# Optimization experiments

Hardware: AMD Instinct MI355X
Metric: run time of the kernel (lower is better)

Reference implementation:

```python
import jax, jax.numpy as jnp
import numpy as np

N = 200000          # graph_size (stalk rows)
H = 128             # hidden_channels
NNZ = 3200000       # Laplacian nnz (avg degree 16)
K = 15              # polynomial degree (poly_layers_K)
LAMBDA_MAX = 2.0    # normalised Laplacian -> analytic lambda_max


def setup_inputs() -> dict:
    key = jax.random.key(0)
    ks = jax.random.split(key, 6)
    x = jax.random.normal(ks[0], (N, H), dtype=jnp.float32)
    vals = jax.random.normal(ks[1], (NNZ,), dtype=jnp.float32)
    poly_logits = jax.random.normal(ks[2], (K + 1,), dtype=jnp.float32)
    hp_alpha = jax.random.normal(ks[3], (), dtype=jnp.float32)
    edge_row = jax.random.randint(ks[4], (NNZ,), 0, N, dtype=jnp.int64)
    edge_col = jax.random.randint(ks[5], (NNZ,), 0, N, dtype=jnp.int64)
    return {"x": x, "vals": vals, "poly_logits": poly_logits,
            "hp_alpha": hp_alpha, "edge_row": edge_row, "edge_col": edge_col}


def reference(x, vals, poly_logits, hp_alpha, edge_row, edge_col):
    n = x.shape[0]

    def spmm(v):  # (n,h) -> (n,h), sparse L @ v in COO form
        return jax.ops.segment_sum(vals[:, None] * v[edge_col], edge_row,
                                   num_segments=n)

    def Lhat(v):  # L_hat = (2/lambda_max) L - I
        return (2.0 / LAMBDA_MAX) * spmm(v) - v

    w = jax.nn.softmax(poly_logits)  # mixture over Chebyshev T_0..T_K

    # Chebyshev Type-1 recurrence: T_{k+1} = 2 L_hat T_k - T_{k-1}
    T0 = x
    T1 = Lhat(x)
    out = w[0] * T0 + w[1] * T1

    def step(carry, wk):
        T0, T1, out = carry
        Tk1 = 2.0 * Lhat(T1) - T0
        return (T1, Tk1, out + wk * Tk1), None

    (_, _, px), _ = jax.lax.scan(step, (T0, T1, out), w[2:])

    # high-pass term: x - (1/lambda_max) L x
    hp = x - spmm(x) / LAMBDA_MAX
    return -px + hp_alpha * hp
```

## Files before the change

kernel.cpp:

```cpp
#include <hip/hip_runtime.h>
#include <math.h>

#define N_NODES 200000
#define H_CH    128
#define GRP     64
#define NNZ_E   3200000
#define K_DEG   15

#define EPB     4096
#define BSHIFT  9
#define BROWS   512
#define NBUCK   391
#define BCAP    9216

__global__ void softmax_k(const float* __restrict__ logits, float* __restrict__ w) {
    if (threadIdx.x == 0) {
        float m = -1e30f;
        for (int i = 0; i <= K_DEG; ++i) m = fmaxf(m, logits[i]);
        float e[K_DEG + 1];
        float s = 0.f;
        for (int i = 0; i <= K_DEG; ++i) { e[i] = expf(logits[i] - m); s += e[i]; }
        float inv = 1.0f / s;
        for (int i = 0; i <= K_DEG; ++i) w[i] = e[i] * inv;
    }
}

__global__ __launch_bounds__(256) void bucketA_k(
    const int* __restrict__ row, const int* __restrict__ col,
    const float* __restrict__ vals,
    int* __restrict__ gfill, uint2* __restrict__ stag, int nnz) {
    __shared__ int cnt[NBUCK];
    __shared__ int excl[NBUCK];
    __shared__ int gbase[NBUCK];
    __shared__ int sm[256];
    __shared__ uint2 sstag[EPB];
    __shared__ unsigned short sb[EPB];

    int tid = threadIdx.x;
    int base = blockIdx.x * EPB;

    for (int t = tid; t < NBUCK; t += 256) cnt[t] = 0;
    __syncthreads();

    int r[16], c[16], b[16];
    float v[16];
#pragma unroll
    for (int j = 0; j < 16; ++j) {
        int i = base + j * 256 + tid;
        if (i < nnz) {
            r[j] = row[i]; c[j] = col[i]; v[j] = vals[i];
            b[j] = r[j] >> BSHIFT;
            atomicAdd(&cnt[b[j]], 1);
        } else {
            b[j] = -1;
        }
    }
    __syncthreads();

    {
        int b0 = 2 * tid, b1 = 2 * tid + 1;
        int c0 = (b0 < NBUCK) ? cnt[b0] : 0;
        int c1 = (b1 < NBUCK) ? cnt[b1] : 0;
        int pair = c0 + c1;
        sm[tid] = pair;
        __syncthreads();
        int incl = pair;
        for (int off = 1; off < 256; off <<= 1) {
            int tv = (tid >= off) ? sm[tid - off] : 0;
            __syncthreads();
            incl += tv;
            sm[tid] = incl;
            __syncthreads();
        }
        int pexcl = incl - pair;
        if (b0 < NBUCK) excl[b0] = pexcl;
        if (b1 < NBUCK) excl[b1] = pexcl + c0;
    }
    __syncthreads();

    for (int t = tid; t < NBUCK; t += 256) {
        int cb = cnt[t];
        gbase[t] = (cb > 0) ? atomicAdd(&gfill[t], cb) : 0;
    }
    __syncthreads();
    for (int t = tid; t < NBUCK; t += 256) cnt[t] = excl[t];
    __syncthreads();

#pragma unroll
    for (int j = 0; j < 16; ++j) {
        if (b[j] >= 0) {
            int p = atomicAdd(&cnt[b[j]], 1);
            sstag[p] = make_uint2(((unsigned)(r[j] & 511) << 18) | (unsigned)c[j],
                                  __float_as_uint(v[j]));
            sb[p] = (unsigned short)b[j];
        }
    }
    __syncthreads();

    int tot = nnz - base; if (tot > EPB) tot = EPB;
    for (int i = tid; i < tot; i += 256) {
        int bb = sb[i];
        size_t gp = (size_t)bb * BCAP + gbase[bb] + (i - excl[bb]);
        stag[gp] = sstag[i];
    }
}

__global__ void scanG_k(const int* __restrict__ gfill, int* __restrict__ bbase,
                        int* __restrict__ row_ptr) {
    __shared__ int sm[256];
    int tid = threadIdx.x;
    int j0 = 2 * tid, j1 = 2 * tid + 1;
    int c0 = (j0 < NBUCK) ? gfill[j0] : 0;
    int c1 = (j1 < NBUCK) ? gfill[j1] : 0;
    int pair = c0 + c1;
    sm[tid] = pair;
    __syncthreads();
    int incl = pair;
    for (int off = 1; off < 256; off <<= 1) {
        int t = (tid >= off) ? sm[tid - off] : 0;
        __syncthreads();
        incl += t;
        sm[tid] = incl;
        __syncthreads();
    }
    int pexcl = incl - pair;
    if (j0 < NBUCK) bbase[j0] = pexcl;
    if (j1 < NBUCK) bbase[j1] = pexcl + c0;
    if (tid == 0) row_ptr[N_NODES] = NNZ_E;
}

__global__ __launch_bounds__(256) void bucketB_k(
    const uint2* __restrict__ stag, const int* __restrict__ gfill,
    const int* __restrict__ bbase, int* __restrict__ row_ptr,
    int2* __restrict__ csr) {
    __shared__ int hist[BROWS];
    __shared__ int lexcl[BROWS];
    __shared__ int sm[256];
    int b = blockIdx.x;
    int n = gfill[b];
    int cs = bbase[b];
    const uint2* s = stag + (size_t)b * BCAP;
    int tid = threadIdx.x;

    hist[tid] = 0; hist[tid + 256] = 0;
    __syncthreads();
    for (int i = tid; i < n; i += 256)
        atomicAdd(&hist[s[i].x >> 18], 1);
    __syncthreads();

    int j0 = 2 * tid, j1 = 2 * tid + 1;
    int c0 = hist[j0], c1 = hist[j1];
    int pair = c0 + c1;
    sm[tid] = pair;
    __syncthreads();
    int incl = pair;
    for (int off = 1; off < 256; off <<= 1) {
        int t = (tid >= off) ? sm[tid - off] : 0;
        __syncthreads();
        incl += t;
        sm[tid] = incl;
        __syncthreads();
    }
    int pexcl = incl - pair;
    lexcl[j0] = pexcl;
    lexcl[j1] = pexcl + c0;

    int rbase = b << BSHIFT;
    if (rbase + j0 < N_NODES) row_ptr[rbase + j0] = cs + lexcl[j0];
    if (rbase + j1 < N_NODES) row_ptr[rbase + j1] = cs + lexcl[j1];
    hist[j0] = lexcl[j0];
    hist[j1] = lexcl[j1];
    __syncthreads();

    for (int i = tid; i < n; i += 256) {
        uint2 e = s[i];
        int rl = (int)(e.x >> 18);
        int p = cs + atomicAdd(&hist[rl], 1);
        int2 cv;
        cv.x = (int)(e.x & 0x3FFFF);
        cv.y = (int)e.y;
        csr[p] = cv;
    }
}

__global__ __launch_bounds__(256) void first_k(
    const int* __restrict__ rp, const int2* __restrict__ csr,
    const float* __restrict__ x, float* __restrict__ T1g, float* __restrict__ out,
    const float* __restrict__ w, const float* __restrict__ alpha_p, int goff) {
    int wid = blockIdx.x * 4 + (threadIdx.x >> 6);
    int r = __builtin_amdgcn_readfirstlane(wid);
    if (r >= N_NODES) return;
    int lane = threadIdx.x & 63;
    const float* base = x + goff + lane;
    int e0 = rp[r], e1 = rp[r + 1];
    float a0 = 0.f, a1 = 0.f, a2 = 0.f, a3 = 0.f;
    int e = e0;
    for (; e + 4 <= e1; e += 4) {
        int2 cv0 = csr[e], cv1 = csr[e + 1], cv2 = csr[e + 2], cv3 = csr[e + 3];
        a0 = fmaf(__int_as_float(cv0.y), base[(size_t)cv0.x * H_CH], a0);
        a1 = fmaf(__int_as_float(cv1.y), base[(size_t)cv1.x * H_CH], a1);
        a2 = fmaf(__int_as_float(cv2.y), base[(size_t)cv2.x * H_CH], a2);
        a3 = fmaf(__int_as_float(cv3.y), base[(size_t)cv3.x * H_CH], a3);
    }
    for (; e < e1; ++e) {
        int2 cv = csr[e];
        a0 = fmaf(__int_as_float(cv.y), base[(size_t)cv.x * H_CH], a0);
    }
    float s = (a0 + a1) + (a2 + a3);
    size_t idxg = (size_t)r * GRP + lane;
    size_t idxf = (size_t)r * H_CH + goff + lane;
    float xr = x[idxf];
    float w0 = w[0], w1 = w[1], al = alpha_p[0];
    float t1 = s - xr;
    float o = -(w0 * xr + w1 * t1) + al * (xr - 0.5f * s);
    T1g[idxg] = t1;
    out[idxf] = o;
}

__global__ __launch_bounds__(256) void cheb_k(
    const int* __restrict__ rp, const int2* __restrict__ csr,
    const float* __restrict__ Tcur, const float* TprevBase, int tprevStride,
    float* Tnext, float* __restrict__ out,
    const float* __restrict__ w, int k, int goff) {
    int wid = blockIdx.x * 4 + (threadIdx.x >> 6);
    int r = __builtin_amdgcn_readfirstlane(wid);
    if (r >= N_NODES) return;
    int lane = threadIdx.x & 63;
    const float* base = Tcur + lane;
    int e0 = rp[r], e1 = rp[r + 1];
    float a0 = 0.f, a1 = 0.f, a2 = 0.f, a3 = 0.f;
    int e = e0;
    for (; e + 4 <= e1; e += 4) {
        int2 cv0 = csr[e], cv1 = csr[e + 1], cv2 = csr[e + 2], cv3 = csr[e + 3];
        a0 = fmaf(__int_as_float(cv0.y), base[(size_t)cv0.x * GRP], a0);
        a1 = fmaf(__int_as_float(cv1.y), base[(size_t)cv1.x * GRP], a1);
        a2 = fmaf(__int_as_float(cv2.y), base[(size_t)cv2.x * GRP], a2);
        a3 = fmaf(__int_as_float(cv3.y), base[(size_t)cv3.x * GRP], a3);
    }
    for (; e < e1; ++e) {
        int2 cv = csr[e];
        a0 = fmaf(__int_as_float(cv.y), base[(size_t)cv.x * GRP], a0);
    }
    float s = (a0 + a1) + (a2 + a3);
    size_t idxg = (size_t)r * GRP + lane;
    size_t idxf = (size_t)r * H_CH + goff + lane;
    float tc = Tcur[idxg];
    float tp = TprevBase[(size_t)r * tprevStride + lane];
    float wk = w[k];
    float tn = 2.0f * (s - tc) - tp;
    float o = out[idxf];
    o -= wk * tn;
    out[idxf] = o;
    Tnext[idxg] = tn;
}

extern "C" void kernel_launch(void* const* d_in, const int* in_sizes, int n_in,
                              void* d_out, int out_size, void* d_ws, size_t ws_size,
                              hipStream_t stream) {
    const float* x      = (const float*)d_in[0];
    const float* vals   = (const float*)d_in[1];
    const float* logits = (const float*)d_in[2];
    const float* alpha  = (const float*)d_in[3];
    const int*   erow   = (const int*)d_in[4];
    const int*   ecol   = (const int*)d_in[5];
    float* out = (float*)d_out;

    const size_t NG = (size_t)N_NODES * GRP;
    float* bufA    = (float*)d_ws;
    float* bufB    = bufA + NG;
    int2*  csr     = (int2*)(bufB + NG);
    uint2* stag    = (uint2*)(csr + NNZ_E);
    int*   row_ptr = (int*)(stag + (size_t)NBUCK * BCAP);
    int*   gfill   = row_ptr + (N_NODES + 1);
    int*   bbase   = gfill + NBUCK;
    float* w_buf   = (float*)(bbase + NBUCK);

    hipMemsetAsync(gfill, 0, NBUCK * sizeof(int), stream);
    softmax_k<<<1, 64, 0, stream>>>(logits, w_buf);

    int nblkA = (NNZ_E + EPB - 1) / EPB;
    bucketA_k<<<nblkA, 256, 0, stream>>>(erow, ecol, vals, gfill, stag, NNZ_E);
    scanG_k<<<1, 256, 0, stream>>>(gfill, bbase, row_ptr);
    bucketB_k<<<NBUCK, 256, 0, stream>>>(stag, gfill, bbase, row_ptr, csr);

    int grid = (N_NODES + 3) / 4;

    for (int g = 0; g < H_CH / GRP; ++g) {
        int goff = g * GRP;
        first_k<<<grid, 256, 0, stream>>>(row_ptr, csr, x, bufB, out, w_buf, alpha, goff);
        cheb_k<<<grid, 256, 0, stream>>>(row_ptr, csr, bufB, x + goff, H_CH, bufA,
                                         out, w_buf, 2, goff);
        float* Tcur = bufA;
        float* Tprev = bufB;
        for (int k = 3; k <= K_DEG; ++k) {
            cheb_k<<<grid, 256, 0, stream>>>(row_ptr, csr, Tcur, Tprev, GRP, Tprev,
                                             out, w_buf, k, goff);
            float* t = Tcur; Tcur = Tprev; Tprev = t;
        }
    }
}
```

Baseline: 4.429 ms.

## Fuse Chebyshev iterations into persistent kernel with grid-wide atomic barriers

Replaces the 30 separate first_k/cheb_k launches with one persistent kernel of 768 blocks. Each wave owns a fixed set of rows, keeps the output accumulator in registers across all polynomial steps, and writes out once per channel group. Steps are separated by a software grid barrier built on an atomic counter. This removes launch overhead and the per-step read-modify-write of out, but adds barrier spin cost and high register pressure (66 accumulators per lane). It also relies on all 768 blocks being co-resident, or the barrier deadlocks.

```diff
diff --git a/kernel.cpp b/kernel.cpp
--- a/kernel.cpp
+++ b/kernel.cpp
@@ -12,6 +12,10 @@
 #define BROWS   512
 #define NBUCK   391
 #define BCAP    9216
+
+#define PBLK    768
+#define PWAVES  (PBLK * 4)
+#define RPW     66
 
 __global__ void softmax_k(const float* __restrict__ logits, float* __restrict__ w) {
     if (threadIdx.x == 0) {
@@ -183,75 +187,103 @@
     }
 }
 
-__global__ __launch_bounds__(256) void first_k(
+__device__ __forceinline__ void gsync(int* cnt, int target) {
+    __syncthreads();
+    if (threadIdx.x == 0) {
+        __hip_atomic_fetch_add(cnt, 1, __ATOMIC_RELEASE, __HIP_MEMORY_SCOPE_AGENT);
+        while (__hip_atomic_load(cnt, __ATOMIC_RELAXED, __HIP_MEMORY_SCOPE_AGENT) < target)
+            __builtin_amdgcn_s_sleep(2);
+        __threadfence();
+    }
+    __syncthreads();
+}
+
+__global__ __launch_bounds__(256, 4) void poly_k(
     const int* __restrict__ rp, const int2* __restrict__ csr,
-    const float* __restrict__ x, float* __restrict__ T1g, float* __restrict__ out,
-    const float* __restrict__ w, const float* __restrict__ alpha_p, int goff) {
-    int wid = blockIdx.x * 4 + (threadIdx.x >> 6);
-    int r = __builtin_amdgcn_readfirstlane(wid);
-    if (r >= N_NODES) return;
-    int lane = threadIdx.x & 63;
-    const float* base = x + goff + lane;
-    int e0 = rp[r], e1 = rp[r + 1];
-    float a0 = 0.f, a1 = 0.f, a2 = 0.f, a3 = 0.f;
-    int e = e0;
-    for (; e + 4 <= e1; e += 4) {
-        int2 cv0 = csr[e], cv1 = csr[e + 1], cv2 = csr[e + 2], cv3 = csr[e + 3];
-        a0 = fmaf(__int_as_float(cv0.y), base[(size_t)cv0.x * H_CH], a0);
-        a1 = fmaf(__int_as_float(cv1.y), base[(size_t)cv1.x * H_CH], a1);
-        a2 = fmaf(__int_as_float(cv2.y), base[(size_t)cv2.x * H_CH], a2);
-        a3 = fmaf(__int_as_float(cv3.y), base[(size_t)cv3.x * H_CH], a3);
-    }
-    for (; e < e1; ++e) {
-        int2 cv = csr[e];
-        a0 = fmaf(__int_as_float(cv.y), base[(size_t)cv.x * H_CH], a0);
-    }
-    float s = (a0 + a1) + (a2 + a3);
-    size_t idxg = (size_t)r * GRP + lane;
-    size_t idxf = (size_t)r * H_CH + goff + lane;
-    float xr = x[idxf];
-    float w0 = w[0], w1 = w[1], al = alpha_p[0];
-    float t1 = s - xr;
-    float o = -(w0 * xr + w1 * t1) + al * (xr - 0.5f * s);
-    T1g[idxg] = t1;
-    out[idxf] = o;
-}
-
-__global__ __launch_bounds__(256) void cheb_k(
-    const int* __restrict__ rp, const int2* __restrict__ csr,
-    const float* __restrict__ Tcur, const float* TprevBase, int tprevStride,
-    float* Tnext, float* __restrict__ out,
-    const float* __restrict__ w, int k, int goff) {
-    int wid = blockIdx.x * 4 + (threadIdx.x >> 6);
-    int r = __builtin_amdgcn_readfirstlane(wid);
-    if (r >= N_NODES) return;
-    int lane = threadIdx.x & 63;
-    const float* base = Tcur + lane;
-    int e0 = rp[r], e1 = rp[r + 1];
-    float a0 = 0.f, a1 = 0.f, a2 = 0.f, a3 = 0.f;
-    int e = e0;
-    for (; e + 4 <= e1; e += 4) {
-        int2 cv0 = csr[e], cv1 = csr[e + 1], cv2 = csr[e + 2], cv3 = csr[e + 3];
-        a0 = fmaf(__int_as_float(cv0.y), base[(size_t)cv0.x * GRP], a0);
-        a1 = fmaf(__int_as_float(cv1.y), base[(size_t)cv1.x * GRP], a1);
-        a2 = fmaf(__int_as_float(cv2.y), base[(size_t)cv2.x * GRP], a2);
-        a3 = fmaf(__int_as_float(cv3.y), base[(size_t)cv3.x * GRP], a3);
-    }
-    for (; e < e1; ++e) {
-        int2 cv = csr[e];
-        a0 = fmaf(__int_as_float(cv.y), base[(size_t)cv.x * GRP], a0);
-    }
-    float s = (a0 + a1) + (a2 + a3);
-    size_t idxg = (size_t)r * GRP + lane;
-    size_t idxf = (size_t)r * H_CH + goff + lane;
-    float tc = Tcur[idxg];
-    float tp = TprevBase[(size_t)r * tprevStride + lane];
-    float wk = w[k];
-    float tn = 2.0f * (s - tc) - tp;
-    float o = out[idxf];
-    o -= wk * tn;
-    out[idxf] = o;
-    Tnext[idxg] = tn;
+    const float* __restrict__ x, float* __restrict__ bufA,
+    float* __restrict__ bufB, float* __restrict__ out,
+    const float* __restrict__ w, const float* __restrict__ alpha_p,
+    int* __restrict__ barcnt) {
+    const int tid = threadIdx.x;
+    const int wv = __builtin_amdgcn_readfirstlane(blockIdx.x * 4 + (tid >> 6));
+    const int lane = tid & 63;
+    const float w0 = w[0], w1 = w[1], al = alpha_p[0];
+    float oa[RPW];
+    int gen = 0;
+
+    for (int g = 0; g < 2; ++g) {
+        const int goff = g << 6;
+
+#pragma unroll
+        for (int j = 0; j < RPW; ++j) {
+            const int r = wv + PWAVES * j;
+            if (r < N_NODES) {
+                const float* gb = x + goff + lane;
+                const int e0 = rp[r], e1 = rp[r + 1];
+                float a0 = 0.f, a1 = 0.f, a2 = 0.f, a3 = 0.f;
+                int e = e0;
+                for (; e + 4 <= e1; e += 4) {
+                    int2 c0 = csr[e], c1 = csr[e + 1], c2 = csr[e + 2], c3 = csr[e + 3];
+                    a0 = fmaf(__int_as_float(c0.y), gb[(unsigned)c0.x * H_CH], a0);
+                    a1 = fmaf(__int_as_float(c1.y), gb[(unsigned)c1.x * H_CH], a1);
+                    a2 = fmaf(__int_as_float(c2.y), gb[(unsigned)c2.x * H_CH], a2);
+                    a3 = fmaf(__int_as_float(c3.y), gb[(unsigned)c3.x * H_CH], a3);
+                }
+                for (; e < e1; ++e) {
+                    int2 cv = csr[e];
+                    a0 = fmaf(__int_as_float(cv.y), gb[(unsigned)cv.x * H_CH], a0);
+                }
+                float s = (a0 + a1) + (a2 + a3);
+                float xr = x[(unsigned)r * H_CH + goff + lane];
+                float t1 = s - xr;
+                bufB[(unsigned)r * GRP + lane] = t1;
+                oa[j] = -(w0 * xr + w1 * t1) + al * (xr - 0.5f * s);
+            }
+        }
+        gsync(barcnt, (++gen) * PBLK);
+
+        for (int k = 2; k <= K_DEG; ++k) {
+            const float* Tc = (k & 1) ? bufA : bufB;
+            float* Tn = (k & 1) ? bufB : bufA;
+            const float wk = w[k];
+#pragma unroll
+            for (int j = 0; j < RPW; ++j) {
+                const int r = wv + PWAVES * j;
+                if (r < N_NODES) {
+                    const float* gb = Tc + lane;
+                    const int e0 = rp[r], e1 = rp[r + 1];
+                    float a0 = 0.f, a1 = 0.f, a2 = 0.f, a3 = 0.f;
+                    int e = e0;
+                    for (; e + 4 <= e1; e += 4) {
+                        int2 c0 = csr[e], c1 = csr[e + 1], c2 = csr[e + 2], c3 = csr[e + 3];
+                        a0 = fmaf(__int_as_float(c0.y), gb[(unsigned)c0.x * GRP], a0);
+                        a1 = fmaf(__int_as_float(c1.y), gb[(unsigned)c1.x * GRP], a1);
+                        a2 = fmaf(__int_as_float(c2.y), gb[(unsigned)c2.x * GRP], a2);
+                        a3 = fmaf(__int_as_float(c3.y), gb[(unsigned)c3.x * GRP], a3);
+                    }
+                    for (; e < e1; ++e) {
+                        int2 cv = csr[e];
+                        a0 = fmaf(__int_as_float(cv.y), gb[(unsigned)cv.x * GRP], a0);
+                    }
+                    float s = (a0 + a1) + (a2 + a3);
+                    const unsigned idxg = (unsigned)r * GRP + lane;
+                    float tc = Tc[idxg];
+                    float tp = (k == 2) ? x[(unsigned)r * H_CH + goff + lane]
+                                        : Tn[idxg];
+                    float tn = 2.0f * (s - tc) - tp;
+                    Tn[idxg] = tn;
+                    oa[j] -= wk * tn;
+                }
+            }
+            gsync(barcnt, (++gen) * PBLK);
+        }
+
+#pragma unroll
+        for (int j = 0; j < RPW; ++j) {
+            const int r = wv + PWAVES * j;
+            if (r < N_NODES) out[(unsigned)r * H_CH + goff + lane] = oa[j];
+        }
+    }
 }
 
 extern "C" void kernel_launch(void* const* d_in, const int* in_sizes, int n_in,
@@ -274,8 +306,10 @@
     int*   gfill   = row_ptr + (N_NODES + 1);
     int*   bbase   = gfill + NBUCK;
     float* w_buf   = (float*)(bbase + NBUCK);
+    int*   barcnt  = (int*)(w_buf + 16);
 
     hipMemsetAsync(gfill, 0, NBUCK * sizeof(int), stream);
+    hipMemsetAsync(barcnt, 0, sizeof(int), stream);
     softmax_k<<<1, 64, 0, stream>>>(logits, w_buf);
 
     int nblkA = (NNZ_E + EPB - 1) / EPB;
@@ -283,19 +317,6 @@
     scanG_k<<<1, 256, 0, stream>>>(gfill, bbase, row_ptr);
     bucketB_k<<<NBUCK, 256, 0, stream>>>(stag, gfill, bbase, row_ptr, csr);
 
-    int grid = (N_NODES + 3) / 4;
-
-    for (int g = 0; g < H_CH / GRP; ++g) {
-        int goff = g * GRP;
-        first_k<<<grid, 256, 0, stream>>>(row_ptr, csr, x, bufB, out, w_buf, alpha, goff);
-        cheb_k<<<grid, 256, 0, stream>>>(row_ptr, csr, bufB, x + goff, H_CH, bufA,
-                                         out, w_buf, 2, goff);
-        float* Tcur = bufA;
-        float* Tprev = bufB;
-        for (int k = 3; k <= K_DEG; ++k) {
-            cheb_k<<<grid, 256, 0, stream>>>(row_ptr, csr, Tcur, Tprev, GRP, Tprev,
-                                             out, w_buf, k, goff);
-            float* t = Tcur; Tcur = Tprev; Tprev = t;
-        }
-    }
-}
+    poly_k<<<PBLK, 256, 0, stream>>>(row_ptr, csr, x, bufA, bufB, out,
+                                     w_buf, alpha, barcnt);
+}
```

New measurement: 13.31 ms. 3x slower.

## Process all 128 channels per row pass and pair output updates across steps

Applied to the files above, without the earlier changes.

Replaces the two 64-channel group passes with one pass over the full 128 channels, so the CSR index and value stream is read once per Chebyshev step instead of twice. Each wavefront now handles two 64-float halves per neighbour, and blocks grow to 512 threads. Output accumulation is done only on odd steps, folding in both T_{k-1} and T_k, which halves read-modify-write traffic on out. T buffers become full width, so the staging area is aliased onto bufA to save workspace, and the per-step gather working set doubles, which may hurt cache hit rates.

```diff
diff --git a/kernel.cpp b/kernel.cpp
--- a/kernel.cpp
+++ b/kernel.cpp
@@ -3,7 +3,6 @@
 
 #define N_NODES 200000
 #define H_CH    128
-#define GRP     64
 #define NNZ_E   3200000
 #define K_DEG   15
 
@@ -183,75 +182,97 @@
     }
 }
 
-__global__ __launch_bounds__(256) void first_k(
+__global__ __launch_bounds__(512) void first2_k(
     const int* __restrict__ rp, const int2* __restrict__ csr,
-    const float* __restrict__ x, float* __restrict__ T1g, float* __restrict__ out,
-    const float* __restrict__ w, const float* __restrict__ alpha_p, int goff) {
-    int wid = blockIdx.x * 4 + (threadIdx.x >> 6);
+    const float* __restrict__ x, float* __restrict__ T1, float* __restrict__ out,
+    const float* __restrict__ w, const float* __restrict__ alpha_p) {
+    int wid = blockIdx.x * 8 + (threadIdx.x >> 6);
     int r = __builtin_amdgcn_readfirstlane(wid);
     if (r >= N_NODES) return;
     int lane = threadIdx.x & 63;
-    const float* base = x + goff + lane;
+    const float* g0 = x + lane;
+    const float* g1 = x + 64 + lane;
     int e0 = rp[r], e1 = rp[r + 1];
     float a0 = 0.f, a1 = 0.f, a2 = 0.f, a3 = 0.f;
+    float b0 = 0.f, b1 = 0.f, b2 = 0.f, b3 = 0.f;
     int e = e0;
     for (; e + 4 <= e1; e += 4) {
         int2 cv0 = csr[e], cv1 = csr[e + 1], cv2 = csr[e + 2], cv3 = csr[e + 3];
-        a0 = fmaf(__int_as_float(cv0.y), base[(size_t)cv0.x * H_CH], a0);
-        a1 = fmaf(__int_as_float(cv1.y), base[(size_t)cv1.x * H_CH], a1);
-        a2 = fmaf(__int_as_float(cv2.y), base[(size_t)cv2.x * H_CH], a2);
-        a3 = fmaf(__int_as_float(cv3.y), base[(size_t)cv3.x * H_CH], a3);
+        unsigned o0 = (unsigned)cv0.x * H_CH, o1 = (unsigned)cv1.x * H_CH;
+        unsigned o2 = (unsigned)cv2.x * H_CH, o3 = (unsigned)cv3.x * H_CH;
+        float v0 = __int_as_float(cv0.y), v1 = __int_as_float(cv1.y);
+        float v2 = __int_as_float(cv2.y), v3 = __int_as_float(cv3.y);
+        a0 = fmaf(v0, g0[o0], a0);  b0 = fmaf(v0, g1[o0], b0);
+        a1 = fmaf(v1, g0[o1], a1);  b1 = fmaf(v1, g1[o1], b1);
+        a2 = fmaf(v2, g0[o2], a2);  b2 = fmaf(v2, g1[o2], b2);
+        a3 = fmaf(v3, g0[o3], a3);  b3 = fmaf(v3, g1[o3], b3);
     }
     for (; e < e1; ++e) {
         int2 cv = csr[e];
-        a0 = fmaf(__int_as_float(cv.y), base[(size_t)cv.x * H_CH], a0);
-    }
-    float s = (a0 + a1) + (a2 + a3);
-    size_t idxg = (size_t)r * GRP + lane;
-    size_t idxf = (size_t)r * H_CH + goff + lane;
-    float xr = x[idxf];
+        unsigned o = (unsigned)cv.x * H_CH;
+        float v = __int_as_float(cv.y);
+        a0 = fmaf(v, g0[o], a0);  b0 = fmaf(v, g1[o], b0);
+    }
+    float s0 = (a0 + a1) + (a2 + a3);
+    float s1 = (b0 + b1) + (b2 + b3);
+    size_t idx0 = (size_t)r * H_CH + lane;
+    size_t idx1 = idx0 + 64;
+    float xr0 = x[idx0], xr1 = x[idx1];
     float w0 = w[0], w1 = w[1], al = alpha_p[0];
-    float t1 = s - xr;
-    float o = -(w0 * xr + w1 * t1) + al * (xr - 0.5f * s);
-    T1g[idxg] = t1;
-    out[idxf] = o;
-}
-
-__global__ __launch_bounds__(256) void cheb_k(
+    float t10 = s0 - xr0, t11 = s1 - xr1;
+    T1[idx0] = t10;
+    T1[idx1] = t11;
+    out[idx0] = -(w0 * xr0 + w1 * t10) + al * (xr0 - 0.5f * s0);
+    out[idx1] = -(w0 * xr1 + w1 * t11) + al * (xr1 - 0.5f * s1);
+}
+
+__global__ __launch_bounds__(512) void cheb2_k(
     const int* __restrict__ rp, const int2* __restrict__ csr,
-    const float* __restrict__ Tcur, const float* TprevBase, int tprevStride,
+    const float* __restrict__ Tcur, const float* Tprev,
     float* Tnext, float* __restrict__ out,
-    const float* __restrict__ w, int k, int goff) {
-    int wid = blockIdx.x * 4 + (threadIdx.x >> 6);
+    const float* __restrict__ w, int k) {
+    int wid = blockIdx.x * 8 + (threadIdx.x >> 6);
     int r = __builtin_amdgcn_readfirstlane(wid);
     if (r >= N_NODES) return;
     int lane = threadIdx.x & 63;
-    const float* base = Tcur + lane;
+    const float* g0 = Tcur + lane;
+    const float* g1 = Tcur + 64 + lane;
     int e0 = rp[r], e1 = rp[r + 1];
     float a0 = 0.f, a1 = 0.f, a2 = 0.f, a3 = 0.f;
+    float b0 = 0.f, b1 = 0.f, b2 = 0.f, b3 = 0.f;
     int e = e0;
     for (; e + 4 <= e1; e += 4) {
         int2 cv0 = csr[e], cv1 = csr[e + 1], cv2 = csr[e + 2], cv3 = csr[e + 3];
-        a0 = fmaf(__int_as_float(cv0.y), base[(size_t)cv0.x * GRP], a0);
-        a1 = fmaf(__int_as_float(cv1.y), base[(size_t)cv1.x * GRP], a1);
-        a2 = fmaf(__int_as_float(cv2.y), base[(size_t)cv2.x * GRP], a2);
-        a3 = fmaf(__int_as_float(cv3.y), base[(size_t)cv3.x * GRP], a3);
+        unsigned o0 = (unsigned)cv0.x * H_CH, o1 = (unsigned)cv1.x * H_CH;
+        unsigned o2 = (unsigned)cv2.x * H_CH, o3 = (unsigned)cv3.x * H_CH;
+        float v0 = __int_as_float(cv0.y), v1 = __int_as_float(cv1.y);
+        float v2 = __int_as_float(cv2.y), v3 = __int_as_float(cv3.y);
+        a0 = fmaf(v0, g0[o0], a0);  b0 = fmaf(v0, g1[o0], b0);
+        a1 = fmaf(v1, g0[o1], a1);  b1 = fmaf(v1, g1[o1], b1);
+        a2 = fmaf(v2, g0[o2], a2);  b2 = fmaf(v2, g1[o2], b2);
+        a3 = fmaf(v3, g0[o3], a3);  b3 = fmaf(v3, g1[o3], b3);
     }
     for (; e < e1; ++e) {
         int2 cv = csr[e];
-        a0 = fmaf(__int_as_float(cv.y), base[(size_t)cv.x * GRP], a0);
-    }
-    float s = (a0 + a1) + (a2 + a3);
-    size_t idxg = (size_t)r * GRP + lane;
-    size_t idxf = (size_t)r * H_CH + goff + lane;
-    float tc = Tcur[idxg];
-    float tp = TprevBase[(size_t)r * tprevStride + lane];
-    float wk = w[k];
-    float tn = 2.0f * (s - tc) - tp;
-    float o = out[idxf];
-    o -= wk * tn;
-    out[idxf] = o;
-    Tnext[idxg] = tn;
+        unsigned o = (unsigned)cv.x * H_CH;
+        float v = __int_as_float(cv.y);
+        a0 = fmaf(v, g0[o], a0);  b0 = fmaf(v, g1[o], b0);
+    }
+    float s0 = (a0 + a1) + (a2 + a3);
+    float s1 = (b0 + b1) + (b2 + b3);
+    size_t idx0 = (size_t)r * H_CH + lane;
+    size_t idx1 = idx0 + 64;
+    float tc0 = Tcur[idx0], tc1 = Tcur[idx1];
+    float tp0 = Tprev[idx0], tp1 = Tprev[idx1];
+    float tn0 = 2.0f * (s0 - tc0) - tp0;
+    float tn1 = 2.0f * (s1 - tc1) - tp1;
+    Tnext[idx0] = tn0;
+    Tnext[idx1] = tn1;
+    if (k & 1) {
+        float wk = w[k], wkm1 = w[k - 1];
+        out[idx0] -= wkm1 * tc0 + wk * tn0;
+        out[idx1] -= wkm1 * tc1 + wk * tn1;
+    }
 }
 
 extern "C" void kernel_launch(void* const* d_in, const int* in_sizes, int n_in,
@@ -265,12 +286,12 @@
     const int*   ecol   = (const int*)d_in[5];
     float* out = (float*)d_out;
 
-    const size_t NG = (size_t)N_NODES * GRP;
+    const size_t NF = (size_t)N_NODES * H_CH;
     float* bufA    = (float*)d_ws;
-    float* bufB    = bufA + NG;
-    int2*  csr     = (int2*)(bufB + NG);
-    uint2* stag    = (uint2*)(csr + NNZ_E);
-    int*   row_ptr = (int*)(stag + (size_t)NBUCK * BCAP);
+    float* bufB    = bufA + NF;
+    int2*  csr     = (int2*)(bufB + NF);
+    uint2* stag    = (uint2*)bufA;
+    int*   row_ptr = (int*)(csr + NNZ_E);
     int*   gfill   = row_ptr + (N_NODES + 1);
     int*   bbase   = gfill + NBUCK;
     float* w_buf   = (float*)(bbase + NBUCK);
@@ -283,19 +304,15 @@
     scanG_k<<<1, 256, 0, stream>>>(gfill, bbase, row_ptr);
     bucketB_k<<<NBUCK, 256, 0, stream>>>(stag, gfill, bbase, row_ptr, csr);
 
-    int grid = (N_NODES + 3) / 4;
-
-    for (int g = 0; g < H_CH / GRP; ++g) {
-        int goff = g * GRP;
-        first_k<<<grid, 256, 0, stream>>>(row_ptr, csr, x, bufB, out, w_buf, alpha, goff);
-        cheb_k<<<grid, 256, 0, stream>>>(row_ptr, csr, bufB, x + goff, H_CH, bufA,
-                                         out, w_buf, 2, goff);
-        float* Tcur = bufA;
-        float* Tprev = bufB;
-        for (int k = 3; k <= K_DEG; ++k) {
-            cheb_k<<<grid, 256, 0, stream>>>(row_ptr, csr, Tcur, Tprev, GRP, Tprev,
-                                             out, w_buf, k, goff);
-            float* t = Tcur; Tcur = Tprev; Tprev = t;
-        }
-    }
-}
+    int grid = (N_NODES + 7) / 8;
+
+    first2_k<<<grid, 512, 0, stream>>>(row_ptr, csr, x, bufB, out, w_buf, alpha);
+    cheb2_k<<<grid, 512, 0, stream>>>(row_ptr, csr, bufB, x, bufA, out, w_buf, 2);
+    float* Tcur = bufA;
+    float* Tprev = bufB;
+    for (int k = 3; k <= K_DEG; ++k) {
+        cheb2_k<<<grid, 512, 0, stream>>>(row_ptr, csr, Tcur, Tprev, Tprev,
+                                          out, w_buf, k);
+        float* t = Tcur; Tcur = Tprev; Tprev = t;
+    }
+}
```

After: 4.372 ms. About the same (-1.3%).
